# Performance work log

Hardware: AMD Instinct MI355X
Metric: run time of the kernel (lower is better)

## Reference

```python
import jax, jax.numpy as jnp
import numpy as np

# rendering_options baked in: clamp_mode='softplus', given_bg=False,
# given_bg_dino=True, black_bg_dino=False

def setup_inputs() -> dict:
    key = jax.random.key(0)
    k1, k2, k3, k4 = jax.random.split(key, 4)
    B, R, S, C, Cd = 2, 16384, 48, 32, 64
    colors = jax.random.uniform(k1, (B, R, S, C), dtype=jnp.float32)
    densities = jax.random.normal(k2, (B, R, S, 1), dtype=jnp.float32)
    # sorted depths per ray in [0.5, 2.0] so deltas are positive
    depths = jnp.sort(
        jax.random.uniform(k3, (B, R, S, 1), dtype=jnp.float32) * 1.5 + 0.5,
        axis=2)
    dinos = jax.random.uniform(k4, (B, R, S, Cd), dtype=jnp.float32)
    return {"colors": colors, "densities": densities, "depths": depths, "dinos": dinos}


def reference(colors, densities, depths, dinos):
    deltas = depths[:, :, 1:] - depths[:, :, :-1]          # [B,R,S-1,1]
    colors_mid = (colors[:, :, :-1] + colors[:, :, 1:]) * 0.5
    densities_mid = (densities[:, :, :-1] + densities[:, :, 1:]) * 0.5
    depths_mid = (depths[:, :, :-1] + depths[:, :, 1:]) * 0.5
    dinos_mid = (dinos[:, :, :-1] + dinos[:, :, 1:]) * 0.5

    densities_mid = jax.nn.softplus(densities_mid - 1.0)   # clamp_mode='softplus'
    density_delta = densities_mid * deltas
    alpha = 1.0 - jnp.exp(-density_delta)                  # [B,R,S-1,1]

    alpha_shifted = jnp.concatenate(
        [jnp.ones_like(alpha[:, :, :1]), 1.0 - alpha + 1e-10], axis=-2)
    T = jnp.cumprod(alpha_shifted, axis=-2)[:, :, :-1]     # transmittance [B,R,S-1,1]
    weights = alpha * T

    composite_rgb = jnp.sum(weights * colors_mid, axis=-2)          # [B,R,C]
    weight_total = jnp.sum(weights, axis=2)                         # [B,R,1]
    composite_depth = jnp.sum(weights * depths_mid, axis=-2) / weight_total
    composite_dino = jnp.sum(weights * dinos_mid, axis=-2)          # [B,R,Cd]

    mean_depth = jnp.sum(weights * depths_mid, axis=-2, keepdims=True)
    var_depth = jnp.sum(weights * (depths_mid - mean_depth) ** 2, axis=-2) / (weight_total + 1e-6)
    var_depth = jnp.mean(var_depth)

    composite_depth = jnp.nan_to_num(composite_depth, nan=jnp.inf)
    composite_depth = jnp.clip(composite_depth, jnp.min(depths), jnp.max(depths))

    # given_bg=False -> rgb unchanged; given_bg_dino=True, black_bg_dino=False:
    composite_dino = composite_dino + 1.0 - weight_total

    composite_rgb = composite_rgb * 2.0 - 1.0
    composite_dino = composite_dino * 2.0 - 1.0

    bg_lambda = T[:, :, -1]                                 # [B,R,1]
    return (composite_rgb, composite_depth, weights, bg_lambda,
            composite_dino, weight_total, var_depth)
```

## Files before the change

kernel.cpp:

```cpp
#include <hip/hip_runtime.h>
#include <math.h>

#define NB 2
#define NR 16384
#define NRAY (NB*NR)
#define NS 48
#define NC 32
#define ND 64
#define NBLK (NRAY/4)


__global__ void init_ws_kernel(unsigned int* ws) {
    ws[0] = 0x7f7fffffu;
    ws[1] = 0u;
}

__global__ void minmax_kernel(const float* __restrict__ depths, unsigned int* __restrict__ ws) {
    int ray = blockIdx.x * blockDim.x + threadIdx.x;
    float mn = depths[(size_t)ray * NS];
    float mx = depths[(size_t)ray * NS + (NS - 1)];
#pragma unroll
    for (int off = 32; off > 0; off >>= 1) {
        mn = fminf(mn, __shfl_xor(mn, off));
        mx = fmaxf(mx, __shfl_xor(mx, off));
    }
    if ((threadIdx.x & 63) == 0) {
        atomicMin(&ws[0], __float_as_uint(mn));
        atomicMax(&ws[1], __float_as_uint(mx));
    }
}

__device__ __forceinline__ float4 shfl_xor4(float4 v, int m) {
    float4 r;
    r.x = __shfl_xor(v.x, m);
    r.y = __shfl_xor(v.y, m);
    r.z = __shfl_xor(v.z, m);
    r.w = __shfl_xor(v.w, m);
    return r;
}

__global__ __launch_bounds__(256) void march_kernel(
    const float* __restrict__ colors, const float* __restrict__ densities,
    const float* __restrict__ depths, const float* __restrict__ dinos,
    float* __restrict__ out, const unsigned int* __restrict__ ws_mm,
    float* __restrict__ vb)
{
    const int wid  = threadIdx.x >> 6;
    const int lane = threadIdx.x & 63;
    const int ray  = blockIdx.x * 4 + wid;

    __shared__ float v_sh[4][NS];
    __shared__ float var_sh[4];

    const float* dep = depths    + (size_t)ray * NS;
    const float* den = densities + (size_t)ray * NS;

    float d_i = (lane < NS) ? dep[lane] : 0.f;
    float n_i = (lane < NS) ? den[lane] : 0.f;
    float d_n = __shfl_down(d_i, 1);
    float n_n = __shfl_down(n_i, 1);

    const bool act = (lane < NS - 1);
    float delta = d_n - d_i;
    float dm    = 0.5f * (d_i + d_n);
    float x     = 0.5f * (n_i + n_n) - 1.0f;
    float sp    = fmaxf(x, 0.f) + log1pf(expf(-fabsf(x)));
    float alpha = act ? (1.f - expf(-sp * delta)) : 0.f;
    float f     = act ? (1.f - alpha + 1e-10f) : 1.f;

    float incl = f;
#pragma unroll
    for (int off = 1; off < 64; off <<= 1) {
        float o = __shfl_up(incl, off);
        if (lane >= off) incl *= o;
    }
    float T = __shfl_up(incl, 1);
    if (lane == 0) T = 1.f;
    float w  = alpha * T;
    float bg = __shfl(incl, 45);

    float W = w, M = w * dm;
#pragma unroll
    for (int off = 32; off > 0; off >>= 1) {
        W += __shfl_xor(W, off);
        M += __shfl_xor(M, off);
    }
    float dv = dm - M;
    float vn = w * dv * dv;
#pragma unroll
    for (int off = 32; off > 0; off >>= 1) vn += __shfl_xor(vn, off);

    float wprev = __shfl_up(w, 1);
    if (lane == 0) wprev = 0.f;
    float v = 0.5f * (wprev + w);
    if (lane < NS) v_sh[wid][lane] = v;

    float* out_rgb = out;
    float* out_dep = out + (size_t)NRAY * NC;
    float* out_w   = out + (size_t)NRAY * (NC + 1);
    float* out_bg  = out + (size_t)NRAY * (NC + 1 + (NS - 1));
    float* out_din = out + (size_t)NRAY * (NC + 2 + (NS - 1));
    float* out_wt  = out + (size_t)NRAY * (NC + 2 + (NS - 1) + ND);

    if (act) out_w[(size_t)ray * (NS - 1) + lane] = w;

    if (lane == 0) {
        float cd = M / W;
        if (cd != cd) cd = INFINITY;
        float gmin = __uint_as_float(ws_mm[0]);
        float gmax = __uint_as_float(ws_mm[1]);
        cd = fminf(fmaxf(cd, gmin), gmax);
        out_dep[ray] = cd;
        out_bg[ray]  = bg;
        out_wt[ray]  = W;
        var_sh[wid]  = vn / (W + 1e-6f);
    }

    {
        const float4* cp = (const float4*)(colors + (size_t)ray * (NS * NC));
        const int jr = lane >> 3;
        float4 acc = make_float4(0.f, 0.f, 0.f, 0.f);
#pragma unroll
        for (int t = 0; t < NS / 8; ++t) {
            float vv = v_sh[wid][8 * t + jr];
            float4 c = cp[64 * t + lane];
            acc.x += vv * c.x; acc.y += vv * c.y; acc.z += vv * c.z; acc.w += vv * c.w;
        }
#pragma unroll
        for (int off = 8; off < 64; off <<= 1) {
            float4 o = shfl_xor4(acc, off);
            acc.x += o.x; acc.y += o.y; acc.z += o.z; acc.w += o.w;
        }
        if (lane < 8) {
            float4 r = make_float4(2.f * acc.x - 1.f, 2.f * acc.y - 1.f,
                                   2.f * acc.z - 1.f, 2.f * acc.w - 1.f);
            ((float4*)(out_rgb + (size_t)ray * NC))[lane] = r;
        }
    }

    {
        const float4* dp = (const float4*)(dinos + (size_t)ray * (NS * ND));
        const int jr = lane >> 4;
        float4 acc = make_float4(0.f, 0.f, 0.f, 0.f);
#pragma unroll
        for (int t = 0; t < NS / 4; ++t) {
            float vv = v_sh[wid][4 * t + jr];
            float4 c = dp[64 * t + lane];
            acc.x += vv * c.x; acc.y += vv * c.y; acc.z += vv * c.z; acc.w += vv * c.w;
        }
#pragma unroll
        for (int off = 16; off < 64; off <<= 1) {
            float4 o = shfl_xor4(acc, off);
            acc.x += o.x; acc.y += o.y; acc.z += o.z; acc.w += o.w;
        }
        if (lane < 16) {
            float b = 1.f - 2.f * W;
            float4 r = make_float4(2.f * acc.x + b, 2.f * acc.y + b,
                                   2.f * acc.z + b, 2.f * acc.w + b);
            ((float4*)(out_din + (size_t)ray * ND))[lane] = r;
        }
    }

    __syncthreads();
    if (threadIdx.x == 0) {
        vb[blockIdx.x] = var_sh[0] + var_sh[1] + var_sh[2] + var_sh[3];
    }
}

__global__ __launch_bounds__(256) void finalize_kernel(
    const float* __restrict__ vb, float* __restrict__ out)
{
    float s = 0.f;
    for (int i = threadIdx.x; i < NBLK; i += 256) s += vb[i];
#pragma unroll
    for (int off = 32; off > 0; off >>= 1) s += __shfl_xor(s, off);
    __shared__ float sh[4];
    if ((threadIdx.x & 63) == 0) sh[threadIdx.x >> 6] = s;
    __syncthreads();
    if (threadIdx.x == 0)
        out[(size_t)NRAY * 146] = (sh[0] + sh[1] + sh[2] + sh[3]) * (1.0f / (float)NRAY);
}

extern "C" void kernel_launch(void* const* d_in, const int* in_sizes, int n_in,
                              void* d_out, int out_size, void* d_ws, size_t ws_size,
                              hipStream_t stream) {
    const float* colors    = (const float*)d_in[0];
    const float* densities = (const float*)d_in[1];
    const float* depths    = (const float*)d_in[2];
    const float* dinos     = (const float*)d_in[3];
    float* out = (float*)d_out;
    unsigned int* ws = (unsigned int*)d_ws;
    float* vb = (float*)ws + 4;

    hipLaunchKernelGGL(init_ws_kernel, dim3(1), dim3(1), 0, stream, ws);
    hipLaunchKernelGGL(minmax_kernel, dim3(NRAY / 256), dim3(256), 0, stream, depths, ws);
    hipLaunchKernelGGL(march_kernel, dim3(NBLK), dim3(256), 0, stream,
                       colors, densities, depths, dinos, out, ws, vb);
    hipLaunchKernelGGL(finalize_kernel, dim3(1), dim3(256), 0, stream, (const float*)vb, out);
}
```

Measured before the change: 151.5 us.

## Fuse depth min/max into march kernel and clamp depth in post pass

```diff
diff --git a/kernel.cpp b/kernel.cpp
--- a/kernel.cpp
+++ b/kernel.cpp
@@ -10,26 +10,6 @@
 #define NBLK (NRAY/4)
 
 
-__global__ void init_ws_kernel(unsigned int* ws) {
-    ws[0] = 0x7f7fffffu;
-    ws[1] = 0u;
-}
-
-__global__ void minmax_kernel(const float* __restrict__ depths, unsigned int* __restrict__ ws) {
-    int ray = blockIdx.x * blockDim.x + threadIdx.x;
-    float mn = depths[(size_t)ray * NS];
-    float mx = depths[(size_t)ray * NS + (NS - 1)];
-#pragma unroll
-    for (int off = 32; off > 0; off >>= 1) {
-        mn = fminf(mn, __shfl_xor(mn, off));
-        mx = fmaxf(mx, __shfl_xor(mx, off));
-    }
-    if ((threadIdx.x & 63) == 0) {
-        atomicMin(&ws[0], __float_as_uint(mn));
-        atomicMax(&ws[1], __float_as_uint(mx));
-    }
-}
-
 __device__ __forceinline__ float4 shfl_xor4(float4 v, int m) {
     float4 r;
     r.x = __shfl_xor(v.x, m);
@@ -42,8 +22,8 @@
 __global__ __launch_bounds__(256) void march_kernel(
     const float* __restrict__ colors, const float* __restrict__ densities,
     const float* __restrict__ depths, const float* __restrict__ dinos,
-    float* __restrict__ out, const unsigned int* __restrict__ ws_mm,
-    float* __restrict__ vb)
+    float* __restrict__ out, float* __restrict__ vb,
+    float* __restrict__ bmn, float* __restrict__ bmx)
 {
     const int wid  = threadIdx.x >> 6;
     const int lane = threadIdx.x & 63;
@@ -51,6 +31,7 @@
 
     __shared__ float v_sh[4][NS];
     __shared__ float var_sh[4];
+    __shared__ float mn_sh[4], mx_sh[4];
 
     const float* dep = depths    + (size_t)ray * NS;
     const float* den = densities + (size_t)ray * NS;
@@ -68,6 +49,9 @@
     float alpha = act ? (1.f - expf(-sp * delta)) : 0.f;
     float f     = act ? (1.f - alpha + 1e-10f) : 1.f;
 
+    if (lane == 0) mn_sh[wid] = d_i;
+    if (lane == NS - 1) mx_sh[wid] = d_i;
+
     float incl = f;
 #pragma unroll
     for (int off = 1; off < 64; off <<= 1) {
@@ -107,9 +91,6 @@
     if (lane == 0) {
         float cd = M / W;
         if (cd != cd) cd = INFINITY;
-        float gmin = __uint_as_float(ws_mm[0]);
-        float gmax = __uint_as_float(ws_mm[1]);
-        cd = fminf(fmaxf(cd, gmin), gmax);
         out_dep[ray] = cd;
         out_bg[ray]  = bg;
         out_wt[ray]  = W;
@@ -163,22 +144,57 @@
 
     __syncthreads();
     if (threadIdx.x == 0) {
-        vb[blockIdx.x] = var_sh[0] + var_sh[1] + var_sh[2] + var_sh[3];
-    }
-}
-
-__global__ __launch_bounds__(256) void finalize_kernel(
-    const float* __restrict__ vb, float* __restrict__ out)
+        vb[blockIdx.x]  = var_sh[0] + var_sh[1] + var_sh[2] + var_sh[3];
+        bmn[blockIdx.x] = fminf(fminf(mn_sh[0], mn_sh[1]), fminf(mn_sh[2], mn_sh[3]));
+        bmx[blockIdx.x] = fmaxf(fmaxf(mx_sh[0], mx_sh[1]), fmaxf(mx_sh[2], mx_sh[3]));
+    }
+}
+
+__global__ __launch_bounds__(256) void post_kernel(
+    const float* __restrict__ vb, const float* __restrict__ bmn,
+    const float* __restrict__ bmx, float* __restrict__ out)
 {
-    float s = 0.f;
-    for (int i = threadIdx.x; i < NBLK; i += 256) s += vb[i];
-#pragma unroll
-    for (int off = 32; off > 0; off >>= 1) s += __shfl_xor(s, off);
-    __shared__ float sh[4];
-    if ((threadIdx.x & 63) == 0) sh[threadIdx.x >> 6] = s;
+    const int tid  = threadIdx.x;
+    const int lane = tid & 63;
+    __shared__ float smn[4], smx[4], ssum[4];
+
+    float mn = 3.402823466e+38f, mx = -3.402823466e+38f;
+    const float4* a4 = (const float4*)bmn;
+    const float4* b4 = (const float4*)bmx;
+    for (int i = tid; i < NBLK / 4; i += 256) {
+        float4 a = a4[i], b = b4[i];
+        mn = fminf(mn, fminf(fminf(a.x, a.y), fminf(a.z, a.w)));
+        mx = fmaxf(mx, fmaxf(fmaxf(b.x, b.y), fmaxf(b.z, b.w)));
+    }
+#pragma unroll
+    for (int off = 32; off > 0; off >>= 1) {
+        mn = fminf(mn, __shfl_xor(mn, off));
+        mx = fmaxf(mx, __shfl_xor(mx, off));
+    }
+    if (lane == 0) { smn[tid >> 6] = mn; smx[tid >> 6] = mx; }
     __syncthreads();
-    if (threadIdx.x == 0)
-        out[(size_t)NRAY * 146] = (sh[0] + sh[1] + sh[2] + sh[3]) * (1.0f / (float)NRAY);
+    float gmin = fminf(fminf(smn[0], smn[1]), fminf(smn[2], smn[3]));
+    float gmax = fmaxf(fmaxf(smx[0], smx[1]), fmaxf(smx[2], smx[3]));
+
+    float* out_dep = out + (size_t)NRAY * NC;
+    int i = blockIdx.x * 256 + tid;
+    float cd = out_dep[i];
+    out_dep[i] = fminf(fmaxf(cd, gmin), gmax);
+
+    if (blockIdx.x == 0) {
+        float s = 0.f;
+        const float4* v4 = (const float4*)vb;
+        for (int i2 = tid; i2 < NBLK / 4; i2 += 256) {
+            float4 v = v4[i2];
+            s += (v.x + v.y) + (v.z + v.w);
+        }
+#pragma unroll
+        for (int off = 32; off > 0; off >>= 1) s += __shfl_xor(s, off);
+        if (lane == 0) ssum[tid >> 6] = s;
+        __syncthreads();
+        if (tid == 0)
+            out[(size_t)NRAY * 146] = (ssum[0] + ssum[1] + ssum[2] + ssum[3]) * (1.0f / (float)NRAY);
+    }
 }
 
 extern "C" void kernel_launch(void* const* d_in, const int* in_sizes, int n_in,
@@ -189,12 +205,12 @@
     const float* depths    = (const float*)d_in[2];
     const float* dinos     = (const float*)d_in[3];
     float* out = (float*)d_out;
-    unsigned int* ws = (unsigned int*)d_ws;
-    float* vb = (float*)ws + 4;
-
-    hipLaunchKernelGGL(init_ws_kernel, dim3(1), dim3(1), 0, stream, ws);
-    hipLaunchKernelGGL(minmax_kernel, dim3(NRAY / 256), dim3(256), 0, stream, depths, ws);
+    float* vb  = (float*)d_ws;
+    float* bmn = vb + NBLK;
+    float* bmx = vb + 2 * NBLK;
+
     hipLaunchKernelGGL(march_kernel, dim3(NBLK), dim3(256), 0, stream,
-                       colors, densities, depths, dinos, out, ws, vb);
-    hipLaunchKernelGGL(finalize_kernel, dim3(1), dim3(256), 0, stream, (const float*)vb, out);
-}
+                       colors, densities, depths, dinos, out, vb, bmn, bmx);
+    hipLaunchKernelGGL(post_kernel, dim3(NRAY / 256), dim3(256), 0, stream,
+                       (const float*)vb, (const float*)bmn, (const float*)bmx, out);
+}
```

New measurement: 132.4 us. -12.6%, faster.
